# Kernel optimization log

Hardware: AMD Instinct MI355X
Metric: run time of the kernel (lower is better)

## Reference

```python
import jax, jax.numpy as jnp
import numpy as np

N = 4096
IN_F = 512
OUT_F = 512


def setup_inputs() -> dict:
    key = jax.random.key(0)
    k1, k2, k3, k4 = jax.random.split(key, 4)
    x = jax.random.normal(k1, (N, IN_F), dtype=jnp.float32)
    adj = jax.random.uniform(k2, (N, N), dtype=jnp.float32)
    # linear params (torch nn.Linear default init: U(-1/sqrt(fan_in), 1/sqrt(fan_in)))
    bound = 1.0 / np.sqrt(IN_F)
    W = jax.random.uniform(k3, (OUT_F, IN_F), minval=-bound, maxval=bound, dtype=jnp.float32)
    b = jax.random.uniform(k4, (OUT_F,), minval=-bound, maxval=bound, dtype=jnp.float32)
    return {"x": x, "adj": adj, "W": W, "b": b}


def reference(x, adj, W, b):
    # adj_hat = adj + I
    adj_hat = adj + jnp.eye(adj.shape[0], dtype=adj.dtype)
    # deg is diagonal with 1/sqrt(rowsum); deg @ adj @ deg == d[:,None] * adj * d[None,:]
    d = 1.0 / jnp.sqrt(adj_hat.sum(axis=1))  # [N]
    norm_adj = d[:, None] * adj_hat * d[None, :]  # [N, N]
    h = norm_adj @ x  # [N, in_features]
    return h @ W.T + b  # [N, out_features]
```

## Files before the change

kernel.cpp:

```cpp
#include <hip/hip_runtime.h>
#include <cstdint>

#define NN 4096
#define FF 512

typedef short bf16x8 __attribute__((ext_vector_type(8)));
typedef float f32x4 __attribute__((ext_vector_type(4)));
typedef float f32x16 __attribute__((ext_vector_type(16)));

__device__ __forceinline__ uint16_t f2bf(float f) {
    uint32_t u = __builtin_bit_cast(uint32_t, f);
    u += 0x7FFFu + ((u >> 16) & 1u);
    return (uint16_t)(u >> 16);
}
__device__ __forceinline__ float bf2f(uint32_t h) {
    uint32_t u = h << 16;
    return __builtin_bit_cast(float, u);
}

__global__ __launch_bounds__(256) void k_prep(const float* __restrict__ adj,
                                              float* __restrict__ d,
                                              uint16_t* __restrict__ Abf) {
    const int row  = blockIdx.x * 4 + (threadIdx.x >> 6);
    const int lane = threadIdx.x & 63;
    const float4* p = (const float4*)(adj + (size_t)row * NN);
    float4 v[16];
    float s = 0.f;
#pragma unroll
    for (int i = 0; i < 16; ++i) {
        v[i] = p[lane + i * 64];
        s += (v[i].x + v[i].y) + (v[i].z + v[i].w);
    }
#pragma unroll
    for (int off = 1; off < 64; off <<= 1) s += __shfl_xor(s, off);
    const float di = rsqrtf(s + 1.0f);
    if (lane == 0) d[row] = di;
    uint16_t* outp = Abf + (size_t)row * NN;
#pragma unroll
    for (int i = 0; i < 16; ++i) {
        const int cb = (lane + i * 64) * 4;
        float a0 = v[i].x, a1 = v[i].y, a2 = v[i].z, a3 = v[i].w;
        if (cb + 0 == row) a0 += 1.0f;
        if (cb + 1 == row) a1 += 1.0f;
        if (cb + 2 == row) a2 += 1.0f;
        if (cb + 3 == row) a3 += 1.0f;
        ushort4 o;
        o.x = f2bf(a0); o.y = f2bf(a1); o.z = f2bf(a2); o.w = f2bf(a3);
        *(ushort4*)(outp + cb) = o;
    }
}

__global__ __launch_bounds__(256) void k_xc(const float* __restrict__ x,
                                            uint16_t* __restrict__ xbf) {
    const size_t t4 = (size_t)blockIdx.x * 256 + threadIdx.x;
    float4 v = *(const float4*)(x + t4 * 4);
    ushort4 o;
    o.x = f2bf(v.x); o.y = f2bf(v.y); o.z = f2bf(v.z); o.w = f2bf(v.w);
    *(ushort4*)(xbf + t4 * 4) = o;
}

__global__ __launch_bounds__(256) void k_wc(const float* __restrict__ W,
                                            uint16_t* __restrict__ Wbf) {
    const size_t t4 = (size_t)blockIdx.x * 256 + threadIdx.x;
    float4 v = *(const float4*)(W + t4 * 4);
    ushort4 o;
    o.x = f2bf(v.x); o.y = f2bf(v.y); o.z = f2bf(v.z); o.w = f2bf(v.w);
    *(ushort4*)(Wbf + t4 * 4) = o;
}

__global__ __launch_bounds__(256, 4) void k_mmz(const uint16_t* __restrict__ A,
                                                const uint16_t* __restrict__ Bt,
                                                const float* __restrict__ d,
                                                uint16_t* __restrict__ zdT) {
    constexpr int BM = 64, BN = 64, K = FF;
    constexpr int NTC = FF / BN;
    constexpr int NT  = K / 64;

    __shared__ uint16_t As[BM * 64];
    __shared__ uint16_t Bs[BN * 64];
    __shared__ uint16_t tt[64][80];

    const int id = blockIdx.x;
    const int mt = id / NTC;
    const int nt = id % NTC;
    const int m0 = mt * BM;
    const int n0 = nt * BN;

    const int tid  = threadIdx.x;
    const int w    = tid >> 6;
    const int lane = tid & 63;
    const int wm = w >> 1, wn = w & 1;

    f32x4 acc[2][2] = {};

    for (int t = 0; t < NT; ++t) {
        const int ktb = t * 64;
#pragma unroll
        for (int i = 0; i < 2; ++i) {
            const int boff = i * 4096 + tid * 16;
            const int row  = boff >> 7;
            const int q    = (boff >> 4) & 7;
            const int c    = q ^ (row & 7);
            const uint16_t* src = A + (size_t)(m0 + row) * K + ktb + c * 8;
            __builtin_amdgcn_global_load_lds(
                (const __attribute__((address_space(1))) void*)src,
                (__attribute__((address_space(3))) void*)&As[boff >> 1],
                16, 0, 0);
        }
#pragma unroll
        for (int i = 0; i < 2; ++i) {
            const int boff = i * 4096 + tid * 16;
            const int row  = boff >> 7;
            const int q    = (boff >> 4) & 7;
            const int c    = q ^ (row & 7);
            const uint16_t* src = Bt + (size_t)(n0 + row) * K + ktb + c * 8;
            __builtin_amdgcn_global_load_lds(
                (const __attribute__((address_space(1))) void*)src,
                (__attribute__((address_space(3))) void*)&Bs[boff >> 1],
                16, 0, 0);
        }
        __syncthreads();
#pragma unroll
        for (int kk = 0; kk < 2; ++kk) {
            const int cl = kk * 4 + (lane >> 4);
            bf16x8 af[2], bfr[2];
#pragma unroll
            for (int mf = 0; mf < 2; ++mf) {
                const int r = wm * 32 + mf * 16 + (lane & 15);
                af[mf] = *(const bf16x8*)&As[r * 64 + ((cl ^ (r & 7)) << 3)];
            }
#pragma unroll
            for (int nf = 0; nf < 2; ++nf) {
                const int r = wn * 32 + nf * 16 + (lane & 15);
                bfr[nf] = *(const bf16x8*)&Bs[r * 64 + ((cl ^ (r & 7)) << 3)];
            }
#pragma unroll
            for (int mf = 0; mf < 2; ++mf)
#pragma unroll
                for (int nf = 0; nf < 2; ++nf)
                    acc[mf][nf] = __builtin_amdgcn_mfma_f32_16x16x32_bf16(
                        af[mf], bfr[nf], acc[mf][nf], 0, 0, 0);
        }
        __syncthreads();
    }

    const int rb = wm * 32 + ((lane >> 4) << 2);
    const int cb = wn * 32 + (lane & 15);
#pragma unroll
    for (int mf = 0; mf < 2; ++mf)
#pragma unroll
        for (int nf = 0; nf < 2; ++nf) {
            const int col_l = cb + nf * 16;
#pragma unroll
            for (int r = 0; r < 4; ++r) {
                const int row_l = rb + mf * 16 + r;
                tt[col_l][row_l] = f2bf(acc[mf][nf][r] * d[m0 + row_l]);
            }
        }
    __syncthreads();
    const int n_l = tid >> 2;
    const int ch  = tid & 3;
    uint4* dst = (uint4*)(zdT + (size_t)(n0 + n_l) * NN + m0 + ch * 16);
    dst[0] = *(const uint4*)&tt[n_l][ch * 16];
    dst[1] = *(const uint4*)&tt[n_l][ch * 16 + 8];
}

__global__ __launch_bounds__(512, 2) void k_mmx(const uint16_t* __restrict__ A,
                                                const uint16_t* __restrict__ Bt,
                                                uint16_t* __restrict__ parts) {
    constexpr int BM = 128, BN = 256, K = NN, SPLITK = 8;
    constexpr int KSLEN = K / SPLITK;
    constexpr int NT    = KSLEN / 32;

    __shared__ uint16_t As[2][BM * 32];
    __shared__ uint16_t Bs[2][BN * 32];

    const int id   = blockIdx.x;
    const int xcd  = id & 7;
    const int slot = id >> 3;
    const int mt   = xcd * 4 + (slot >> 4);
    const int rem  = slot & 15;
    const int ks   = rem >> 1;
    const int nt   = rem & 1;
    const int m0 = mt * BM;
    const int n0 = nt * BN;
    const int k0 = ks * KSLEN;

    const int tid  = threadIdx.x;
    const int w    = tid >> 6;
    const int lane = tid & 63;
    const int wm = w >> 2, wn = w & 3;

    f32x16 acc[2][2] = {};

    auto STAGE = [&](int t, int buf) {
        const int ktb = k0 + t * 32;
        {
            const int boff = tid * 16;
            const int row  = boff >> 6;
            const int q    = (boff >> 4) & 3;
            const int c    = q ^ (row & 3);
            const uint16_t* src = A + (size_t)(m0 + row) * K + ktb + c * 8;
            __builtin_amdgcn_global_load_lds(
                (const __attribute__((address_space(1))) void*)src,
                (__attribute__((address_space(3))) void*)&As[buf][boff >> 1],
                16, 0, 0);
        }
#pragma unroll
        for (int i = 0; i < 2; ++i) {
            const int boff = i * 8192 + tid * 16;
            const int row  = boff >> 6;
            const int q    = (boff >> 4) & 3;
            const int c    = q ^ (row & 3);
            const uint16_t* src = Bt + (size_t)(n0 + row) * K + ktb + c * 8;
            __builtin_amdgcn_global_load_lds(
                (const __attribute__((address_space(1))) void*)src,
                (__attribute__((address_space(3))) void*)&Bs[buf][boff >> 1],
                16, 0, 0);
        }
    };

    auto COMPUTE = [&](int buf) {
#pragma unroll
        for (int kk = 0; kk < 2; ++kk) {
            const int cl = kk * 2 + (lane >> 5);
            bf16x8 af[2], bfr[2];
#pragma unroll
            for (int mf = 0; mf < 2; ++mf) {
                const int r = wm * 64 + mf * 32 + (lane & 31);
                af[mf] = *(const bf16x8*)&As[buf][r * 32 + ((cl ^ (r & 3)) << 3)];
            }
#pragma unroll
            for (int nf = 0; nf < 2; ++nf) {
                const int r = wn * 64 + nf * 32 + (lane & 31);
                bfr[nf] = *(const bf16x8*)&Bs[buf][r * 32 + ((cl ^ (r & 3)) << 3)];
            }
#pragma unroll
            for (int mf = 0; mf < 2; ++mf)
#pragma unroll
                for (int nf = 0; nf < 2; ++nf)
                    acc[mf][nf] = __builtin_amdgcn_mfma_f32_32x32x16_bf16(
                        af[mf], bfr[nf], acc[mf][nf], 0, 0, 0);
        }
    };

    STAGE(0, 0);
    for (int t = 0; t < NT - 1; ++t) {
        STAGE(t + 1, (t + 1) & 1);
        asm volatile("s_waitcnt vmcnt(3)" ::: "memory");
        __builtin_amdgcn_s_barrier();
        COMPUTE(t & 1);
        __builtin_amdgcn_s_barrier();
    }
    asm volatile("s_waitcnt vmcnt(0)" ::: "memory");
    __builtin_amdgcn_s_barrier();
    COMPUTE((NT - 1) & 1);

    uint16_t* dst = parts + (size_t)ks * NN * FF;
    const int rb = m0 + wm * 64 + ((lane >> 5) << 2);
    const int cb = n0 + wn * 64 + (lane & 31);
#pragma unroll
    for (int mf = 0; mf < 2; ++mf)
#pragma unroll
        for (int nf = 0; nf < 2; ++nf) {
            const int gcol = cb + nf * 32;
#pragma unroll
            for (int r = 0; r < 16; ++r) {
                const int grow = rb + mf * 32 + (r & 3) + ((r >> 2) << 3);
                dst[(size_t)grow * FF + gcol] = f2bf(acc[mf][nf][r]);
            }
        }
}

__global__ __launch_bounds__(256) void k_red(const uint16_t* __restrict__ parts,
                                             const float* __restrict__ d,
                                             const float* __restrict__ b,
                                             float* __restrict__ out) {
    constexpr size_t STRIDE = (size_t)NN * FF;
    const size_t g   = (size_t)blockIdx.x * 256 + threadIdx.x;
    const int    row = (int)((g * 8) >> 9);
    const int    col = (int)((g * 8) & 511);
    float s[8] = {};
#pragma unroll
    for (int p = 0; p < 8; ++p) {
        ushort4 v0 = *(const ushort4*)(parts + p * STRIDE + g * 8);
        ushort4 v1 = *(const ushort4*)(parts + p * STRIDE + g * 8 + 4);
        s[0] += bf2f(v0.x); s[1] += bf2f(v0.y); s[2] += bf2f(v0.z); s[3] += bf2f(v0.w);
        s[4] += bf2f(v1.x); s[5] += bf2f(v1.y); s[6] += bf2f(v1.z); s[7] += bf2f(v1.w);
    }
    const float di = d[row];
    float4 o0, o1;
    o0.x = s[0] * di + b[col + 0];
    o0.y = s[1] * di + b[col + 1];
    o0.z = s[2] * di + b[col + 2];
    o0.w = s[3] * di + b[col + 3];
    o1.x = s[4] * di + b[col + 4];
    o1.y = s[5] * di + b[col + 5];
    o1.z = s[6] * di + b[col + 6];
    o1.w = s[7] * di + b[col + 7];
    *(float4*)(out + g * 8)     = o0;
    *(float4*)(out + g * 8 + 4) = o1;
}

extern "C" void kernel_launch(void* const* d_in, const int* in_sizes, int n_in,
                              void* d_out, int out_size, void* d_ws, size_t ws_size,
                              hipStream_t stream) {
    const float* x   = (const float*)d_in[0];
    const float* adj = (const float*)d_in[1];
    const float* W   = (const float*)d_in[2];
    const float* b   = (const float*)d_in[3];
    float* out = (float*)d_out;

    char* ws = (char*)d_ws;
    float*    d_    = (float*)ws;
    uint16_t* Abf   = (uint16_t*)(ws + 65536);
    uint16_t* zdT   = Abf + (size_t)NN * NN;
    uint16_t* xbf   = zdT + (size_t)FF * NN;
    uint16_t* Wbf   = xbf + (size_t)NN * FF;
    uint16_t* parts = Wbf + (size_t)FF * FF;

    k_wc<<<FF * FF / 1024, 256, 0, stream>>>(W, Wbf);
    k_xc<<<NN * FF / 1024, 256, 0, stream>>>(x, xbf);
    k_prep<<<NN / 4, 256, 0, stream>>>(adj, d_, Abf);
    k_mmz<<<512, 256, 0, stream>>>(xbf, Wbf, d_, zdT);
    k_mmx<<<512, 512, 0, stream>>>(Abf, zdT, parts);
    k_red<<<NN * FF / 2048, 256, 0, stream>>>(parts, d_, b, out);
}
```

Before: 70.20 us.

## Fuse adjacency bf16 conversion into main GEMM A-tile staging

New measurement: 69.14 us. No clear change (-1.5%).

```diff
diff --git a/kernel.cpp b/kernel.cpp
--- a/kernel.cpp
+++ b/kernel.cpp
@@ -18,36 +18,20 @@
     return __builtin_bit_cast(float, u);
 }
 
-__global__ __launch_bounds__(256) void k_prep(const float* __restrict__ adj,
-                                              float* __restrict__ d,
-                                              uint16_t* __restrict__ Abf) {
+__global__ __launch_bounds__(256) void k_dsum(const float* __restrict__ adj,
+                                              float* __restrict__ d) {
     const int row  = blockIdx.x * 4 + (threadIdx.x >> 6);
     const int lane = threadIdx.x & 63;
     const float4* p = (const float4*)(adj + (size_t)row * NN);
-    float4 v[16];
     float s = 0.f;
 #pragma unroll
     for (int i = 0; i < 16; ++i) {
-        v[i] = p[lane + i * 64];
-        s += (v[i].x + v[i].y) + (v[i].z + v[i].w);
+        float4 v = p[lane + i * 64];
+        s += (v.x + v.y) + (v.z + v.w);
     }
 #pragma unroll
     for (int off = 1; off < 64; off <<= 1) s += __shfl_xor(s, off);
-    const float di = rsqrtf(s + 1.0f);
-    if (lane == 0) d[row] = di;
-    uint16_t* outp = Abf + (size_t)row * NN;
-#pragma unroll
-    for (int i = 0; i < 16; ++i) {
-        const int cb = (lane + i * 64) * 4;
-        float a0 = v[i].x, a1 = v[i].y, a2 = v[i].z, a3 = v[i].w;
-        if (cb + 0 == row) a0 += 1.0f;
-        if (cb + 1 == row) a1 += 1.0f;
-        if (cb + 2 == row) a2 += 1.0f;
-        if (cb + 3 == row) a3 += 1.0f;
-        ushort4 o;
-        o.x = f2bf(a0); o.y = f2bf(a1); o.z = f2bf(a2); o.w = f2bf(a3);
-        *(ushort4*)(outp + cb) = o;
-    }
+    if (lane == 0) d[row] = rsqrtf(s + 1.0f);
 }
 
 __global__ __launch_bounds__(256) void k_xc(const float* __restrict__ x,
@@ -165,7 +149,7 @@
     dst[1] = *(const uint4*)&tt[n_l][ch * 16 + 8];
 }
 
-__global__ __launch_bounds__(512, 2) void k_mmx(const uint16_t* __restrict__ A,
+__global__ __launch_bounds__(512, 2) void k_mmx(const float* __restrict__ adjf,
                                                 const uint16_t* __restrict__ Bt,
                                                 uint16_t* __restrict__ parts) {
     constexpr int BM = 128, BN = 256, K = NN, SPLITK = 8;
@@ -191,35 +175,45 @@
     const int lane = tid & 63;
     const int wm = w >> 2, wn = w & 3;
 
+    const int arow = tid >> 2;
+    const int ac   = tid & 3;
+    const int aq   = ac ^ (arow & 3);
+    const float* asrc = adjf + (size_t)(m0 + arow) * NN + k0 + ac * 8;
+    const int diagbase = (m0 + arow) - k0 - ac * 8;
+
     f32x16 acc[2][2] = {};
-
-    auto STAGE = [&](int t, int buf) {
-        const int ktb = k0 + t * 32;
-        {
-            const int boff = tid * 16;
-            const int row  = boff >> 6;
-            const int q    = (boff >> 4) & 3;
-            const int c    = q ^ (row & 3);
-            const uint16_t* src = A + (size_t)(m0 + row) * K + ktb + c * 8;
-            __builtin_amdgcn_global_load_lds(
-                (const __attribute__((address_space(1))) void*)src,
-                (__attribute__((address_space(3))) void*)&As[buf][boff >> 1],
-                16, 0, 0);
-        }
+    float4 ar0, ar1;
+
+    auto GLB_A = [&](int T) {
+        ar0 = *(const float4*)(asrc + T * 32);
+        ar1 = *(const float4*)(asrc + T * 32 + 4);
+    };
+    auto CVT_WRITE = [&](int T, int buf) {
+        float a[8] = {ar0.x, ar0.y, ar0.z, ar0.w, ar1.x, ar1.y, ar1.z, ar1.w};
+        const int dj = diagbase - T * 32;
+#pragma unroll
+        for (int j = 0; j < 8; ++j) a[j] += (dj == j) ? 1.0f : 0.0f;
+        uint32_t w0 = (uint32_t)f2bf(a[0]) | ((uint32_t)f2bf(a[1]) << 16);
+        uint32_t w1 = (uint32_t)f2bf(a[2]) | ((uint32_t)f2bf(a[3]) << 16);
+        uint32_t w2 = (uint32_t)f2bf(a[4]) | ((uint32_t)f2bf(a[5]) << 16);
+        uint32_t w3 = (uint32_t)f2bf(a[6]) | ((uint32_t)f2bf(a[7]) << 16);
+        uint4 v = {w0, w1, w2, w3};
+        *(uint4*)&As[buf][arow * 32 + aq * 8] = v;
+    };
+    auto GLB_B = [&](int t, int buf) {
 #pragma unroll
         for (int i = 0; i < 2; ++i) {
             const int boff = i * 8192 + tid * 16;
             const int row  = boff >> 6;
             const int q    = (boff >> 4) & 3;
             const int c    = q ^ (row & 3);
-            const uint16_t* src = Bt + (size_t)(n0 + row) * K + ktb + c * 8;
+            const uint16_t* src = Bt + (size_t)(n0 + row) * K + k0 + t * 32 + c * 8;
             __builtin_amdgcn_global_load_lds(
                 (const __attribute__((address_space(1))) void*)src,
                 (__attribute__((address_space(3))) void*)&Bs[buf][boff >> 1],
                 16, 0, 0);
         }
     };
-
     auto COMPUTE = [&](int buf) {
 #pragma unroll
         for (int kk = 0; kk < 2; ++kk) {
@@ -244,12 +238,19 @@
         }
     };
 
-    STAGE(0, 0);
+    GLB_A(0);
+    CVT_WRITE(0, 0);
+    GLB_B(0, 0);
+    GLB_A(1);
     for (int t = 0; t < NT - 1; ++t) {
-        STAGE(t + 1, (t + 1) & 1);
-        asm volatile("s_waitcnt vmcnt(3)" ::: "memory");
+        const int buf = t & 1, nbuf = buf ^ 1;
+        GLB_B(t + 1, nbuf);
+        asm volatile("s_waitcnt vmcnt(2)" ::: "memory");
+        CVT_WRITE(t + 1, nbuf);
+        if (t + 2 < NT) GLB_A(t + 2);
+        asm volatile("s_waitcnt lgkmcnt(0)" ::: "memory");
         __builtin_amdgcn_s_barrier();
-        COMPUTE(t & 1);
+        COMPUTE(buf);
         __builtin_amdgcn_s_barrier();
     }
     asm volatile("s_waitcnt vmcnt(0)" ::: "memory");
@@ -313,16 +314,15 @@
 
     char* ws = (char*)d_ws;
     float*    d_    = (float*)ws;
-    uint16_t* Abf   = (uint16_t*)(ws + 65536);
-    uint16_t* zdT   = Abf + (size_t)NN * NN;
+    uint16_t* zdT   = (uint16_t*)(ws + 65536);
     uint16_t* xbf   = zdT + (size_t)FF * NN;
     uint16_t* Wbf   = xbf + (size_t)NN * FF;
     uint16_t* parts = Wbf + (size_t)FF * FF;
 
     k_wc<<<FF * FF / 1024, 256, 0, stream>>>(W, Wbf);
     k_xc<<<NN * FF / 1024, 256, 0, stream>>>(x, xbf);
-    k_prep<<<NN / 4, 256, 0, stream>>>(adj, d_, Abf);
+    k_dsum<<<NN / 4, 256, 0, stream>>>(adj, d_);
     k_mmz<<<512, 256, 0, stream>>>(xbf, Wbf, d_, zdT);
-    k_mmx<<<512, 512, 0, stream>>>(Abf, zdT, parts);
+    k_mmx<<<512, 512, 0, stream>>>(adj, zdT, parts);
     k_red<<<NN * FF / 2048, 256, 0, stream>>>(parts, d_, b, out);
 }
```

## Merge prep kernels and retile big GEMM to 128x128, split-K 4, K-step 64

Applied to the files above, without the earlier changes.

Result: faster. 57.78 us (median of 2 runs) (-17.7%).

```diff
diff --git a/kernel.cpp b/kernel.cpp
--- a/kernel.cpp
+++ b/kernel.cpp
@@ -18,54 +18,55 @@
     return __builtin_bit_cast(float, u);
 }
 
-__global__ __launch_bounds__(256) void k_prep(const float* __restrict__ adj,
-                                              float* __restrict__ d,
-                                              uint16_t* __restrict__ Abf) {
-    const int row  = blockIdx.x * 4 + (threadIdx.x >> 6);
-    const int lane = threadIdx.x & 63;
-    const float4* p = (const float4*)(adj + (size_t)row * NN);
-    float4 v[16];
-    float s = 0.f;
-#pragma unroll
-    for (int i = 0; i < 16; ++i) {
-        v[i] = p[lane + i * 64];
-        s += (v[i].x + v[i].y) + (v[i].z + v[i].w);
+__global__ __launch_bounds__(256) void k_pre(const float* __restrict__ adj,
+                                             const float* __restrict__ x,
+                                             const float* __restrict__ W,
+                                             float* __restrict__ d,
+                                             uint16_t* __restrict__ Abf,
+                                             uint16_t* __restrict__ xbf,
+                                             uint16_t* __restrict__ Wbf) {
+    const int bid = blockIdx.x;
+    if (bid < 1024) {
+        const int row  = bid * 4 + (threadIdx.x >> 6);
+        const int lane = threadIdx.x & 63;
+        const float4* p = (const float4*)(adj + (size_t)row * NN);
+        float4 v[16];
+        float s = 0.f;
+#pragma unroll
+        for (int i = 0; i < 16; ++i) {
+            v[i] = p[lane + i * 64];
+            s += (v[i].x + v[i].y) + (v[i].z + v[i].w);
+        }
+#pragma unroll
+        for (int off = 1; off < 64; off <<= 1) s += __shfl_xor(s, off);
+        const float di = rsqrtf(s + 1.0f);
+        if (lane == 0) d[row] = di;
+        uint16_t* outp = Abf + (size_t)row * NN;
+#pragma unroll
+        for (int i = 0; i < 16; ++i) {
+            const int cb = (lane + i * 64) * 4;
+            float a0 = v[i].x, a1 = v[i].y, a2 = v[i].z, a3 = v[i].w;
+            if (cb + 0 == row) a0 += 1.0f;
+            if (cb + 1 == row) a1 += 1.0f;
+            if (cb + 2 == row) a2 += 1.0f;
+            if (cb + 3 == row) a3 += 1.0f;
+            ushort4 o;
+            o.x = f2bf(a0); o.y = f2bf(a1); o.z = f2bf(a2); o.w = f2bf(a3);
+            *(ushort4*)(outp + cb) = o;
+        }
+    } else if (bid < 3072) {
+        const size_t t4 = (size_t)(bid - 1024) * 256 + threadIdx.x;
+        float4 v = *(const float4*)(x + t4 * 4);
+        ushort4 o;
+        o.x = f2bf(v.x); o.y = f2bf(v.y); o.z = f2bf(v.z); o.w = f2bf(v.w);
+        *(ushort4*)(xbf + t4 * 4) = o;
+    } else {
+        const size_t t4 = (size_t)(bid - 3072) * 256 + threadIdx.x;
+        float4 v = *(const float4*)(W + t4 * 4);
+        ushort4 o;
+        o.x = f2bf(v.x); o.y = f2bf(v.y); o.z = f2bf(v.z); o.w = f2bf(v.w);
+        *(ushort4*)(Wbf + t4 * 4) = o;
     }
-#pragma unroll
-    for (int off = 1; off < 64; off <<= 1) s += __shfl_xor(s, off);
-    const float di = rsqrtf(s + 1.0f);
-    if (lane == 0) d[row] = di;
-    uint16_t* outp = Abf + (size_t)row * NN;
-#pragma unroll
-    for (int i = 0; i < 16; ++i) {
-        const int cb = (lane + i * 64) * 4;
-        float a0 = v[i].x, a1 = v[i].y, a2 = v[i].z, a3 = v[i].w;
-        if (cb + 0 == row) a0 += 1.0f;
-        if (cb + 1 == row) a1 += 1.0f;
-        if (cb + 2 == row) a2 += 1.0f;
-        if (cb + 3 == row) a3 += 1.0f;
-        ushort4 o;
-        o.x = f2bf(a0); o.y = f2bf(a1); o.z = f2bf(a2); o.w = f2bf(a3);
-        *(ushort4*)(outp + cb) = o;
-    }
-}
-
-__global__ __launch_bounds__(256) void k_xc(const float* __restrict__ x,
-                                            uint16_t* __restrict__ xbf) {
-    const size_t t4 = (size_t)blockIdx.x * 256 + threadIdx.x;
-    float4 v = *(const float4*)(x + t4 * 4);
-    ushort4 o;
-    o.x = f2bf(v.x); o.y = f2bf(v.y); o.z = f2bf(v.z); o.w = f2bf(v.w);
-    *(ushort4*)(xbf + t4 * 4) = o;
-}
-
-__global__ __launch_bounds__(256) void k_wc(const float* __restrict__ W,
-                                            uint16_t* __restrict__ Wbf) {
-    const size_t t4 = (size_t)blockIdx.x * 256 + threadIdx.x;
-    float4 v = *(const float4*)(W + t4 * 4);
-    ushort4 o;
-    o.x = f2bf(v.x); o.y = f2bf(v.y); o.z = f2bf(v.z); o.w = f2bf(v.w);
-    *(ushort4*)(Wbf + t4 * 4) = o;
 }
 
 __global__ __launch_bounds__(256, 4) void k_mmz(const uint16_t* __restrict__ A,
@@ -165,23 +166,25 @@
     dst[1] = *(const uint4*)&tt[n_l][ch * 16 + 8];
 }
 
-__global__ __launch_bounds__(512, 2) void k_mmx(const uint16_t* __restrict__ A,
+__global__ __launch_bounds__(256, 2) void k_mmx(const uint16_t* __restrict__ A,
                                                 const uint16_t* __restrict__ Bt,
                                                 uint16_t* __restrict__ parts) {
-    constexpr int BM = 128, BN = 256, K = NN, SPLITK = 8;
+    constexpr int BM = 128, BN = 128, K = NN, SPLITK = 4;
+    constexpr int NTC   = FF / BN;
     constexpr int KSLEN = K / SPLITK;
-    constexpr int NT    = KSLEN / 32;
-
-    __shared__ uint16_t As[2][BM * 32];
-    __shared__ uint16_t Bs[2][BN * 32];
+    constexpr int NT    = KSLEN / 64;
+    constexpr int MTX   = (NN / BM) / 8;
+
+    __shared__ uint16_t As[2][BM * 64];
+    __shared__ uint16_t Bs[2][BN * 64];
 
     const int id   = blockIdx.x;
     const int xcd  = id & 7;
     const int slot = id >> 3;
-    const int mt   = xcd * 4 + (slot >> 4);
-    const int rem  = slot & 15;
-    const int ks   = rem >> 1;
-    const int nt   = rem & 1;
+    const int mt   = xcd * MTX + slot / (NTC * SPLITK);
+    const int rem  = slot % (NTC * SPLITK);
+    const int nt   = rem % NTC;
+    const int ks   = rem / NTC;
     const int m0 = mt * BM;
     const int n0 = nt * BN;
     const int k0 = ks * KSLEN;
@@ -189,17 +192,18 @@
     const int tid  = threadIdx.x;
     const int w    = tid >> 6;
     const int lane = tid & 63;
-    const int wm = w >> 2, wn = w & 3;
+    const int wm = w >> 1, wn = w & 1;
 
     f32x16 acc[2][2] = {};
 
     auto STAGE = [&](int t, int buf) {
-        const int ktb = k0 + t * 32;
-        {
-            const int boff = tid * 16;
-            const int row  = boff >> 6;
-            const int q    = (boff >> 4) & 3;
-            const int c    = q ^ (row & 3);
+        const int ktb = k0 + t * 64;
+#pragma unroll
+        for (int i = 0; i < 4; ++i) {
+            const int boff = i * 4096 + tid * 16;
+            const int row  = boff >> 7;
+            const int q    = (boff >> 4) & 7;
+            const int c    = q ^ (row & 7);
             const uint16_t* src = A + (size_t)(m0 + row) * K + ktb + c * 8;
             __builtin_amdgcn_global_load_lds(
                 (const __attribute__((address_space(1))) void*)src,
@@ -207,11 +211,11 @@
                 16, 0, 0);
         }
 #pragma unroll
-        for (int i = 0; i < 2; ++i) {
-            const int boff = i * 8192 + tid * 16;
-            const int row  = boff >> 6;
-            const int q    = (boff >> 4) & 3;
-            const int c    = q ^ (row & 3);
+        for (int i = 0; i < 4; ++i) {
+            const int boff = i * 4096 + tid * 16;
+            const int row  = boff >> 7;
+            const int q    = (boff >> 4) & 7;
+            const int c    = q ^ (row & 7);
             const uint16_t* src = Bt + (size_t)(n0 + row) * K + ktb + c * 8;
             __builtin_amdgcn_global_load_lds(
                 (const __attribute__((address_space(1))) void*)src,
@@ -222,18 +226,18 @@
 
     auto COMPUTE = [&](int buf) {
 #pragma unroll
-        for (int kk = 0; kk < 2; ++kk) {
+        for (int kk = 0; kk < 4; ++kk) {
             const int cl = kk * 2 + (lane >> 5);
             bf16x8 af[2], bfr[2];
 #pragma unroll
             for (int mf = 0; mf < 2; ++mf) {
                 const int r = wm * 64 + mf * 32 + (lane & 31);
-                af[mf] = *(const bf16x8*)&As[buf][r * 32 + ((cl ^ (r & 3)) << 3)];
+                af[mf] = *(const bf16x8*)&As[buf][r * 64 + ((cl ^ (r & 7)) << 3)];
             }
 #pragma unroll
             for (int nf = 0; nf < 2; ++nf) {
                 const int r = wn * 64 + nf * 32 + (lane & 31);
-                bfr[nf] = *(const bf16x8*)&Bs[buf][r * 32 + ((cl ^ (r & 3)) << 3)];
+                bfr[nf] = *(const bf16x8*)&Bs[buf][r * 64 + ((cl ^ (r & 7)) << 3)];
             }
 #pragma unroll
             for (int mf = 0; mf < 2; ++mf)
@@ -247,7 +251,7 @@
     STAGE(0, 0);
     for (int t = 0; t < NT - 1; ++t) {
         STAGE(t + 1, (t + 1) & 1);
-        asm volatile("s_waitcnt vmcnt(3)" ::: "memory");
+        asm volatile("s_waitcnt vmcnt(8)" ::: "memory");
         __builtin_amdgcn_s_barrier();
         COMPUTE(t & 1);
         __builtin_amdgcn_s_barrier();
@@ -282,7 +286,7 @@
     const int    col = (int)((g * 8) & 511);
     float s[8] = {};
 #pragma unroll
-    for (int p = 0; p < 8; ++p) {
+    for (int p = 0; p < 4; ++p) {
         ushort4 v0 = *(const ushort4*)(parts + p * STRIDE + g * 8);
         ushort4 v1 = *(const ushort4*)(parts + p * STRIDE + g * 8 + 4);
         s[0] += bf2f(v0.x); s[1] += bf2f(v0.y); s[2] += bf2f(v0.z); s[3] += bf2f(v0.w);
@@ -319,10 +323,8 @@
     uint16_t* Wbf   = xbf + (size_t)NN * FF;
     uint16_t* parts = Wbf + (size_t)FF * FF;
 
-    k_wc<<<FF * FF / 1024, 256, 0, stream>>>(W, Wbf);
-    k_xc<<<NN * FF / 1024, 256, 0, stream>>>(x, xbf);
-    k_prep<<<NN / 4, 256, 0, stream>>>(adj, d_, Abf);
+    k_pre<<<3328, 256, 0, stream>>>(adj, x, W, d_, Abf, xbf, Wbf);
     k_mmz<<<512, 256, 0, stream>>>(xbf, Wbf, d_, zdT);
-    k_mmx<<<512, 512, 0, stream>>>(Abf, zdT, parts);
+    k_mmx<<<512, 256, 0, stream>>>(Abf, zdT, parts);
     k_red<<<NN * FF / 2048, 256, 0, stream>>>(parts, d_, b, out);
 }
```
